# Optimization experiments

Hardware: AMD Instinct MI355X
Metric: run time of the kernel (lower is better)

## Reference

```python
import jax, jax.numpy as jnp
import numpy as np

WEIGHT_GT = 0.004
WEIGHT_BG = 0.0002
STRIDES = (8, 16, 32, 64, 128)
SIZES = (128, 64, 32, 16, 8)
B, C, N = 8, 256, 16


def setup_inputs() -> dict:
    key = jax.random.key(0)
    ks = jax.random.split(key, 32)
    inp = {}
    for i, hw in enumerate(SIZES):
        inp[f"feat_s{i}"] = jax.random.normal(ks[i], (B, C, hw, hw), jnp.float32)
        inp[f"feat_t{i}"] = jax.random.normal(ks[5 + i], (B, C, hw, hw), jnp.float32)
        inp[f"adapt_w{i}"] = jax.random.normal(ks[10 + i], (C, C), jnp.float32) * 0.05
        inp[f"adapt_b{i}"] = jnp.zeros((C,), jnp.float32)
    # valid boxes: x1<x2, y1<y2, inside a 1024px image
    x1 = jax.random.uniform(ks[20], (B, N), minval=0.0, maxval=800.0)
    y1 = jax.random.uniform(ks[21], (B, N), minval=0.0, maxval=800.0)
    bw = jax.random.uniform(ks[22], (B, N), minval=8.0, maxval=224.0)
    bh = jax.random.uniform(ks[23], (B, N), minval=8.0, maxval=224.0)
    inp["gt_bboxes"] = jnp.stack([x1, y1, x1 + bw, y1 + bh], axis=-1)  # [B,N,4]
    return inp


def gt_mask(gt_bboxes, h, w, stride):
    """Vectorized rasterization of the nested-loop mask builder. [B,N,4] -> [B,h,w]."""
    q = jnp.floor(gt_bboxes / stride).astype(jnp.int32)  # int() truncation (coords >= 0)
    lx = jnp.minimum(q[..., 0], w - 1)[:, :, None, None]  # [B,N,1,1]
    ly = jnp.minimum(q[..., 1], h - 1)[:, :, None, None]
    rx = jnp.minimum(q[..., 2], w - 1)[:, :, None, None]
    ry = jnp.minimum(q[..., 3], h - 1)[:, :, None, None]
    Y = jnp.arange(h)[:, None]  # [h,1]
    X = jnp.arange(w)[None, :]  # [1,w]
    degenerate = (lx == rx) | (ly == ry)
    inside = (Y >= ly) & (Y < ry) & (X >= lx) & (X < rx)   # slice ly:ry, lx:rx
    point = (Y == ly) & (X == lx)                          # single-pixel fallback
    per_box = jnp.where(degenerate, point, inside)         # [B,N,h,w]
    return jnp.any(per_box, axis=1).astype(jnp.float32)    # (mask > 0)


def _level_loss(feat_t, feat_s, w, b, gt_bboxes, stride):
    # 1x1-conv adaptation layer
    adapted = jnp.einsum('bchw,oc->bohw', feat_s, w) + b[None, :, None, None]
    h, wd = feat_t.shape[2], feat_t.shape[3]
    mask = gt_mask(gt_bboxes, h, wd, stride)[:, None, :, :]  # [B,1,H,W]
    diff = (feat_t - adapted) ** 2
    s_gt = jnp.sum(diff * mask)
    s_bg = jnp.sum(diff * (1.0 - mask))
    loss_gt = jnp.sqrt(s_gt + 1e-8)
    loss_bg = jnp.sqrt(s_bg + 1e-8)
    return WEIGHT_GT * loss_gt + WEIGHT_BG * loss_bg


def reference(feat_s0, feat_t0, adapt_w0, adapt_b0,
              feat_s1, feat_t1, adapt_w1, adapt_b1,
              feat_s2, feat_t2, adapt_w2, adapt_b2,
              feat_s3, feat_t3, adapt_w3, adapt_b3,
              feat_s4, feat_t4, adapt_w4, adapt_b4,
              gt_bboxes):
    fs = (feat_s0, feat_s1, feat_s2, feat_s3, feat_s4)
    ft = (feat_t0, feat_t1, feat_t2, feat_t3, feat_t4)
    ws = (adapt_w0, adapt_w1, adapt_w2, adapt_w3, adapt_w4)
    bs = (adapt_b0, adapt_b1, adapt_b2, adapt_b3, adapt_b4)
    loss = jnp.float32(0.0)
    for i in range(5):  # fixed, small number of pyramid levels
        loss = loss + _level_loss(ft[i], fs[i], ws[i], bs[i], gt_bboxes, STRIDES[i])
    return loss
```

## Files before the change

kernel.cpp:

```cpp
#include <hip/hip_runtime.h>
#include <math.h>

typedef __attribute__((ext_vector_type(8))) short short8;
typedef __attribute__((ext_vector_type(4))) float floatx4;

__device__ __forceinline__ short f2bf(float f) {
  union { float f; unsigned u; } v; v.f = f;
  unsigned r = v.u + 0x7fffu + ((v.u >> 16) & 1u);
  return (short)(r >> 16);
}

struct Params {
  const float* fs[5];
  const float* ft[5];
  const float* bias[5];
  const float* mask[5];
  const short8* wp[5];
  float* sums;
};

__global__ void prepack_w(const float* __restrict__ w0, const float* __restrict__ w1,
                          const float* __restrict__ w2, const float* __restrict__ w3,
                          const float* __restrict__ w4, short8* __restrict__ wp) {
  int id = blockIdx.x * 256 + threadIdx.x;
  if (id >= 5 * 8192) return;
  int lvl = id >> 13;
  int idx = id & 8191;
  const float* W = (lvl == 0) ? w0 : (lvl == 1) ? w1 : (lvl == 2) ? w2 : (lvl == 3) ? w3 : w4;
  int t16 = idx >> 9;
  int kt  = (idx >> 6) & 7;
  int ln  = idx & 63;
  int m = t16 * 16 + (ln & 15);
  int c = kt * 32 + (ln >> 4) * 8;
  const float* s = W + m * 256 + c;
  short8 v;
#pragma unroll
  for (int j = 0; j < 8; j++) v[j] = f2bf(s[j]);
  wp[id] = v;
}

__global__ void mask_kernel(const float* __restrict__ gtb, float* __restrict__ mask_base) {
  const int szs[5]  = {128, 64, 32, 16, 8};
  const int strd[5] = {8, 16, 32, 64, 128};
  const int offs[5] = {0, 131072, 163840, 172032, 174080};
  int b = blockIdx.x, lvl = blockIdx.y;
  int hw = szs[lvl];
  int P = hw * hw;
  __shared__ int lx[16], ly[16], rx[16], ry[16], dg[16];
  if (threadIdx.x < 16) {
    int n = threadIdx.x;
    const float* bb = gtb + (b * 16 + n) * 4;
    float inv = 1.0f / (float)strd[lvl];
    int qx1 = (int)floorf(bb[0] * inv);
    int qy1 = (int)floorf(bb[1] * inv);
    int qx2 = (int)floorf(bb[2] * inv);
    int qy2 = (int)floorf(bb[3] * inv);
    int wl = hw - 1;
    int a = min(qx1, wl), c = min(qy1, wl), d = min(qx2, wl), e = min(qy2, wl);
    lx[n] = a; ly[n] = c; rx[n] = d; ry[n] = e;
    dg[n] = (a == d) || (c == e);
  }
  __syncthreads();
  float* mp = mask_base + offs[lvl] + b * P;
  for (int p = threadIdx.x; p < P; p += blockDim.x) {
    int y = p / hw, x = p - y * hw;
    bool any = false;
#pragma unroll
    for (int n = 0; n < 16; n++) {
      bool cov = dg[n] ? (y == ly[n] && x == lx[n])
                       : (y >= ly[n] && y < ry[n] && x >= lx[n] && x < rx[n]);
      any = any || cov;
    }
    mp[p] = any ? 1.0f : 0.0f;
  }
}

template<int PL2, int LVL>
__device__ __forceinline__ void level_body(const Params& pr, int rem, float* red) {
  constexpr int P = 64 << PL2;
  const int tid  = threadIdx.x;
  const int lane = tid & 63;
  const int wave = tid >> 6;
  const int quad = lane >> 4, l15 = lane & 15;
  const int bz = rem >> PL2;
  const int p0 = (rem & ((1 << PL2) - 1)) << 6;

  const float*  fsb   = pr.fs[LVL]  + (size_t)bz * 256 * P;
  const float*  ftb   = pr.ft[LVL]  + (size_t)bz * 256 * P;
  const short8* wpb   = pr.wp[LVL]  + (size_t)wave * 4 * 8 * 64;
  const float*  maskb = pr.mask[LVL] + (size_t)bz * P;
  const float*  biasp = pr.bias[LVL];

  floatx4 acc[4][4];
#pragma unroll
  for (int i = 0; i < 4; i++)
#pragma unroll
    for (int j = 0; j < 4; j++) acc[i][j] = (floatx4){0.f, 0.f, 0.f, 0.f};

#pragma unroll 2
  for (int kt = 0; kt < 8; ++kt) {
    short8 af[4];
#pragma unroll
    for (int mi = 0; mi < 4; mi++)
      af[mi] = wpb[(mi * 8 + kt) * 64 + lane];

    short8 bf[4];
#pragma unroll
    for (int ni = 0; ni < 4; ni++) {
      const float* src = fsb + (size_t)(kt * 32 + quad * 8) * P + (p0 + ni * 16 + l15);
      float t[8];
#pragma unroll
      for (int j = 0; j < 8; j++) t[j] = src[(size_t)j * P];
      short8 v;
#pragma unroll
      for (int j = 0; j < 8; j++) v[j] = f2bf(t[j]);
      bf[ni] = v;
    }
#pragma unroll
    for (int mi = 0; mi < 4; mi++)
#pragma unroll
      for (int ni = 0; ni < 4; ni++)
        acc[mi][ni] = __builtin_amdgcn_mfma_f32_16x16x32_bf16(af[mi], bf[ni], acc[mi][ni], 0, 0, 0);
  }

  float sgt = 0.f, sbg = 0.f;
#pragma unroll
  for (int ni = 0; ni < 4; ni++) {
    int p = p0 + ni * 16 + l15;
    float mk = maskb[p];
#pragma unroll
    for (int mi = 0; mi < 4; mi++) {
      int ob = wave * 64 + mi * 16 + quad * 4;
      const float* ftp = ftb + (size_t)ob * P + p;
#pragma unroll
      for (int r = 0; r < 4; r++) {
        float ad = acc[mi][ni][r] + biasp[ob + r];
        float tv = ftp[(size_t)r * P];
        float d = tv - ad;
        float sq = d * d;
        sgt += sq * mk;
        sbg += sq - sq * mk;
      }
    }
  }
#pragma unroll
  for (int off = 32; off > 0; off >>= 1) {
    sgt += __shfl_down(sgt, off);
    sbg += __shfl_down(sbg, off);
  }
  if (lane == 0) { red[wave * 2] = sgt; red[wave * 2 + 1] = sbg; }
  __syncthreads();
  if (tid == 0) {
    atomicAdd(&pr.sums[LVL * 2 + 0], red[0] + red[2] + red[4] + red[6]);
    atomicAdd(&pr.sums[LVL * 2 + 1], red[1] + red[3] + red[5] + red[7]);
  }
}

__global__ __launch_bounds__(256, 2) void gemm_loss_all(Params pr) {
  __shared__ float red[8];
  int id = blockIdx.x;
  if (id < 2048)      level_body<8, 0>(pr, id,        red);
  else if (id < 2560) level_body<6, 1>(pr, id - 2048, red);
  else if (id < 2688) level_body<4, 2>(pr, id - 2560, red);
  else if (id < 2720) level_body<2, 3>(pr, id - 2688, red);
  else                level_body<0, 4>(pr, id - 2720, red);
}

__global__ void finalize(const float* __restrict__ sums, float* __restrict__ out) {
  if (threadIdx.x == 0 && blockIdx.x == 0) {
    float L = 0.f;
#pragma unroll
    for (int i = 0; i < 5; i++)
      L += 0.004f * sqrtf(sums[2 * i] + 1e-8f) + 0.0002f * sqrtf(sums[2 * i + 1] + 1e-8f);
    out[0] = L;
  }
}

extern "C" void kernel_launch(void* const* d_in, const int* in_sizes, int n_in,
                              void* d_out, int out_size, void* d_ws, size_t ws_size,
                              hipStream_t stream) {
  (void)in_sizes; (void)n_in; (void)out_size; (void)ws_size;
  const float* fs[5]; const float* ftp[5]; const float* aw[5]; const float* ab[5];
  for (int i = 0; i < 5; i++) {
    fs[i]  = (const float*)d_in[4 * i + 0];
    ftp[i] = (const float*)d_in[4 * i + 1];
    aw[i]  = (const float*)d_in[4 * i + 2];
    ab[i]  = (const float*)d_in[4 * i + 3];
  }
  const float* gtb = (const float*)d_in[20];
  float* out = (float*)d_out;
  char* ws = (char*)d_ws;

  float*  sums  = (float*)ws;
  float*  masks = (float*)(ws + 64);
  short8* wp    = (short8*)(ws + 64 + 698368);

  hipMemsetAsync(sums, 0, 64, stream);
  prepack_w<<<160, 256, 0, stream>>>(aw[0], aw[1], aw[2], aw[3], aw[4], wp);
  mask_kernel<<<dim3(8, 5), 256, 0, stream>>>(gtb, masks);

  const int moff[5] = {0, 131072, 163840, 172032, 174080};
  Params pr;
  for (int l = 0; l < 5; l++) {
    pr.fs[l]   = fs[l];
    pr.ft[l]   = ftp[l];
    pr.bias[l] = ab[l];
    pr.mask[l] = masks + moff[l];
    pr.wp[l]   = wp + l * 8192;
  }
  pr.sums = sums;

  gemm_loss_all<<<2728, 256, 0, stream>>>(pr);
  finalize<<<1, 64, 0, stream>>>(sums, out);
}
```

Baseline: 457.5 us.

## Stage converted activation tiles in LDS and software-pipeline loads; merge prep kernels

Previously each of the four waves in a block loaded and converted the full 256x64 activation K-slice from global memory on its own, so every load was repeated four times. Now each wave loads only its 16-column share, converts it to bf16 and writes it to a double-buffered LDS tile. All waves then read the full tile from LDS, and the global loads for the next K steps are prefetched two iterations ahead, with a barrier per K step. The weight-prepack, mask and memset launches are also merged into one prep kernel to cut launch count. This adds LDS traffic and a barrier on every iteration, and the extra prefetch registers may cost occupancy.

```diff
diff --git a/kernel.cpp b/kernel.cpp
--- a/kernel.cpp
+++ b/kernel.cpp
@@ -19,64 +19,70 @@
   float* sums;
 };
 
-__global__ void prepack_w(const float* __restrict__ w0, const float* __restrict__ w1,
-                          const float* __restrict__ w2, const float* __restrict__ w3,
-                          const float* __restrict__ w4, short8* __restrict__ wp) {
-  int id = blockIdx.x * 256 + threadIdx.x;
-  if (id >= 5 * 8192) return;
-  int lvl = id >> 13;
-  int idx = id & 8191;
-  const float* W = (lvl == 0) ? w0 : (lvl == 1) ? w1 : (lvl == 2) ? w2 : (lvl == 3) ? w3 : w4;
-  int t16 = idx >> 9;
-  int kt  = (idx >> 6) & 7;
-  int ln  = idx & 63;
-  int m = t16 * 16 + (ln & 15);
-  int c = kt * 32 + (ln >> 4) * 8;
-  const float* s = W + m * 256 + c;
-  short8 v;
-#pragma unroll
-  for (int j = 0; j < 8; j++) v[j] = f2bf(s[j]);
-  wp[id] = v;
-}
-
-__global__ void mask_kernel(const float* __restrict__ gtb, float* __restrict__ mask_base) {
-  const int szs[5]  = {128, 64, 32, 16, 8};
-  const int strd[5] = {8, 16, 32, 64, 128};
-  const int offs[5] = {0, 131072, 163840, 172032, 174080};
-  int b = blockIdx.x, lvl = blockIdx.y;
-  int hw = szs[lvl];
-  int P = hw * hw;
+__global__ void prep(const float* __restrict__ w0, const float* __restrict__ w1,
+                     const float* __restrict__ w2, const float* __restrict__ w3,
+                     const float* __restrict__ w4, short8* __restrict__ wp,
+                     const float* __restrict__ gtb, float* __restrict__ mask_base,
+                     float* __restrict__ sums) {
   __shared__ int lx[16], ly[16], rx[16], ry[16], dg[16];
-  if (threadIdx.x < 16) {
-    int n = threadIdx.x;
-    const float* bb = gtb + (b * 16 + n) * 4;
-    float inv = 1.0f / (float)strd[lvl];
-    int qx1 = (int)floorf(bb[0] * inv);
-    int qy1 = (int)floorf(bb[1] * inv);
-    int qx2 = (int)floorf(bb[2] * inv);
-    int qy2 = (int)floorf(bb[3] * inv);
-    int wl = hw - 1;
-    int a = min(qx1, wl), c = min(qy1, wl), d = min(qx2, wl), e = min(qy2, wl);
-    lx[n] = a; ly[n] = c; rx[n] = d; ry[n] = e;
-    dg[n] = (a == d) || (c == e);
-  }
-  __syncthreads();
-  float* mp = mask_base + offs[lvl] + b * P;
-  for (int p = threadIdx.x; p < P; p += blockDim.x) {
-    int y = p / hw, x = p - y * hw;
-    bool any = false;
-#pragma unroll
-    for (int n = 0; n < 16; n++) {
-      bool cov = dg[n] ? (y == ly[n] && x == lx[n])
-                       : (y >= ly[n] && y < ry[n] && x >= lx[n] && x < rx[n]);
-      any = any || cov;
-    }
-    mp[p] = any ? 1.0f : 0.0f;
+  int blk = blockIdx.x;
+  if (blk < 160) {
+    int id = blk * 256 + threadIdx.x;
+    int lvl = id >> 13;
+    int idx = id & 8191;
+    const float* W = (lvl == 0) ? w0 : (lvl == 1) ? w1 : (lvl == 2) ? w2 : (lvl == 3) ? w3 : w4;
+    int t16 = idx >> 9;
+    int kt  = (idx >> 6) & 7;
+    int ln  = idx & 63;
+    int m = t16 * 16 + (ln & 15);
+    int c = kt * 32 + (ln >> 4) * 8;
+    const float* s = W + m * 256 + c;
+    short8 v;
+#pragma unroll
+    for (int j = 0; j < 8; j++) v[j] = f2bf(s[j]);
+    wp[id] = v;
+  } else if (blk < 200) {
+    const int szs[5]  = {128, 64, 32, 16, 8};
+    const int strd[5] = {8, 16, 32, 64, 128};
+    const int offs[5] = {0, 131072, 163840, 172032, 174080};
+    int idx = blk - 160;
+    int b = idx & 7, lvl = idx >> 3;
+    int hw = szs[lvl];
+    int P = hw * hw;
+    if (threadIdx.x < 16) {
+      int n = threadIdx.x;
+      const float* bb = gtb + (b * 16 + n) * 4;
+      float inv = 1.0f / (float)strd[lvl];
+      int qx1 = (int)floorf(bb[0] * inv);
+      int qy1 = (int)floorf(bb[1] * inv);
+      int qx2 = (int)floorf(bb[2] * inv);
+      int qy2 = (int)floorf(bb[3] * inv);
+      int wl = hw - 1;
+      int a = min(qx1, wl), c = min(qy1, wl), d = min(qx2, wl), e = min(qy2, wl);
+      lx[n] = a; ly[n] = c; rx[n] = d; ry[n] = e;
+      dg[n] = (a == d) || (c == e);
+    }
+    __syncthreads();
+    float* mp = mask_base + offs[lvl] + b * P;
+    for (int p = threadIdx.x; p < P; p += blockDim.x) {
+      int y = p / hw, x = p - y * hw;
+      bool any = false;
+#pragma unroll
+      for (int n = 0; n < 16; n++) {
+        bool cov = dg[n] ? (y == ly[n] && x == lx[n])
+                         : (y >= ly[n] && y < ry[n] && x >= lx[n] && x < rx[n]);
+        any = any || cov;
+      }
+      mp[p] = any ? 1.0f : 0.0f;
+    }
+  } else {
+    if (threadIdx.x < 16) sums[threadIdx.x] = 0.f;
   }
 }
 
 template<int PL2, int LVL>
-__device__ __forceinline__ void level_body(const Params& pr, int rem, float* red) {
+__device__ __forceinline__ void level_body(const Params& pr, int rem, float* red,
+                                           short8 (*lbuf)[64][4]) {
   constexpr int P = 64 << PL2;
   const int tid  = threadIdx.x;
   const int lane = tid & 63;
@@ -87,40 +93,78 @@
 
   const float*  fsb   = pr.fs[LVL]  + (size_t)bz * 256 * P;
   const float*  ftb   = pr.ft[LVL]  + (size_t)bz * 256 * P;
-  const short8* wpb   = pr.wp[LVL]  + (size_t)wave * 4 * 8 * 64;
+  const short8* wpb   = pr.wp[LVL]  + lane;
   const float*  maskb = pr.mask[LVL] + (size_t)bz * P;
   const float*  biasp = pr.bias[LVL];
 
+  const float* gbase = fsb + (size_t)quad * 8 * P + (p0 + wave * 16 + l15);
+
   floatx4 acc[4][4];
 #pragma unroll
   for (int i = 0; i < 4; i++)
 #pragma unroll
     for (int j = 0; j < 4; j++) acc[i][j] = (floatx4){0.f, 0.f, 0.f, 0.f};
 
-#pragma unroll 2
-  for (int kt = 0; kt < 8; ++kt) {
-    short8 af[4];
+  float  g[2][8];
+  short8 af[2][4];
+
+#pragma unroll
+  for (int j = 0; j < 8; j++) g[0][j] = gbase[(size_t)(0 * 32 + j) * P];
+#pragma unroll
+  for (int mi = 0; mi < 4; mi++) af[0][mi] = wpb[((wave * 4 + mi) * 8 + 0) * 64];
+#pragma unroll
+  for (int j = 0; j < 8; j++) g[1][j] = gbase[(size_t)(1 * 32 + j) * P];
+  {
+    short8 v;
+#pragma unroll
+    for (int j = 0; j < 8; j++) v[j] = f2bf(g[0][j]);
+    lbuf[0][wave * 16 + l15][quad] = v;
+  }
+  asm volatile("s_waitcnt lgkmcnt(0)" ::: "memory");
+  __builtin_amdgcn_s_barrier();
+  asm volatile("" ::: "memory");
+
+#pragma unroll
+  for (int kt = 0; kt < 8; kt++) {
+    const int cur = kt & 1;
+    float  gn[8];
+    short8 afn[4];
+    if (kt + 2 < 8) {
+#pragma unroll
+      for (int j = 0; j < 8; j++) gn[j] = gbase[(size_t)((kt + 2) * 32 + j) * P];
+    }
+    if (kt + 1 < 8) {
+#pragma unroll
+      for (int mi = 0; mi < 4; mi++)
+        afn[mi] = wpb[((wave * 4 + mi) * 8 + (kt + 1)) * 64];
+    }
+
+    short8 bf[4];
+#pragma unroll
+    for (int ni = 0; ni < 4; ni++) bf[ni] = lbuf[cur][ni * 16 + l15][quad];
 #pragma unroll
     for (int mi = 0; mi < 4; mi++)
-      af[mi] = wpb[(mi * 8 + kt) * 64 + lane];
-
-    short8 bf[4];
-#pragma unroll
-    for (int ni = 0; ni < 4; ni++) {
-      const float* src = fsb + (size_t)(kt * 32 + quad * 8) * P + (p0 + ni * 16 + l15);
-      float t[8];
-#pragma unroll
-      for (int j = 0; j < 8; j++) t[j] = src[(size_t)j * P];
+#pragma unroll
+      for (int ni = 0; ni < 4; ni++)
+        acc[mi][ni] = __builtin_amdgcn_mfma_f32_16x16x32_bf16(af[cur][mi], bf[ni], acc[mi][ni], 0, 0, 0);
+
+    if (kt + 1 < 8) {
       short8 v;
 #pragma unroll
-      for (int j = 0; j < 8; j++) v[j] = f2bf(t[j]);
-      bf[ni] = v;
-    }
-#pragma unroll
-    for (int mi = 0; mi < 4; mi++)
-#pragma unroll
-      for (int ni = 0; ni < 4; ni++)
-        acc[mi][ni] = __builtin_amdgcn_mfma_f32_16x16x32_bf16(af[mi], bf[ni], acc[mi][ni], 0, 0, 0);
+      for (int j = 0; j < 8; j++) v[j] = f2bf(g[1 - cur][j]);
+      lbuf[1 - cur][wave * 16 + l15][quad] = v;
+#pragma unroll
+      for (int mi = 0; mi < 4; mi++) af[1 - cur][mi] = afn[mi];
+    }
+    if (kt + 2 < 8) {
+#pragma unroll
+      for (int j = 0; j < 8; j++) g[cur][j] = gn[j];
+    }
+    if (kt + 1 < 8) {
+      asm volatile("s_waitcnt lgkmcnt(0)" ::: "memory");
+      __builtin_amdgcn_s_barrier();
+      asm volatile("" ::: "memory");
+    }
   }
 
   float sgt = 0.f, sbg = 0.f;
@@ -157,13 +201,14 @@
 }
 
 __global__ __launch_bounds__(256, 2) void gemm_loss_all(Params pr) {
+  __shared__ short8 lbuf[2][64][4];
   __shared__ float red[8];
   int id = blockIdx.x;
-  if (id < 2048)      level_body<8, 0>(pr, id,        red);
-  else if (id < 2560) level_body<6, 1>(pr, id - 2048, red);
-  else if (id < 2688) level_body<4, 2>(pr, id - 2560, red);
-  else if (id < 2720) level_body<2, 3>(pr, id - 2688, red);
-  else                level_body<0, 4>(pr, id - 2720, red);
+  if (id < 2048)      level_body<8, 0>(pr, id,        red, lbuf);
+  else if (id < 2560) level_body<6, 1>(pr, id - 2048, red, lbuf);
+  else if (id < 2688) level_body<4, 2>(pr, id - 2560, red, lbuf);
+  else if (id < 2720) level_body<2, 3>(pr, id - 2688, red, lbuf);
+  else                level_body<0, 4>(pr, id - 2720, red, lbuf);
 }
 
 __global__ void finalize(const float* __restrict__ sums, float* __restrict__ out) {
@@ -195,9 +240,7 @@
   float*  masks = (float*)(ws + 64);
   short8* wp    = (short8*)(ws + 64 + 698368);
 
-  hipMemsetAsync(sums, 0, 64, stream);
-  prepack_w<<<160, 256, 0, stream>>>(aw[0], aw[1], aw[2], aw[3], aw[4], wp);
-  mask_kernel<<<dim3(8, 5), 256, 0, stream>>>(gtb, masks);
+  prep<<<201, 256, 0, stream>>>(aw[0], aw[1], aw[2], aw[3], aw[4], wp, gtb, masks, sums);
 
   const int moff[5] = {0, 131072, 163840, 172032, 174080};
   Params pr;
```

New measurement: 444.9 us. -2.7%, faster.
